# Kernel optimization log

Measured on AMD Instinct MI355X. Metric: run time of the kernel, lower is better.

Reference implementation:

```python
import jax, jax.numpy as jnp
import numpy as np

N = 500_000   # total nodes across the batch of graphs
D = 256       # node feature dim
G = 4096      # number of graphs (segments)


def setup_inputs() -> dict:
    key = jax.random.key(0)
    k1, k2, k3 = jax.random.split(key, 3)
    x = jax.random.normal(k1, (N, D), dtype=jnp.float32)
    batch = jnp.sort(jax.random.randint(k2, (N,), 0, G, dtype=jnp.int64))
    Wg = jax.random.normal(k3, (D,), dtype=jnp.float32) * (1.0 / np.sqrt(D))
    bg = jnp.zeros((1,), dtype=jnp.float32)
    return {"x": x, "batch": batch, "Wg": Wg, "bg": bg}


def reference(x, batch, Wg, bg):
    # gate_nn: Linear(D, 1), then squeeze -> [N]
    gate = x @ Wg + bg[0]
    # scatter_softmax over segments defined by batch
    gmax = jax.ops.segment_max(gate, batch, num_segments=G, indices_are_sorted=True)
    e = jnp.exp(gate - gmax[batch])
    denom = jax.ops.segment_sum(e, batch, num_segments=G, indices_are_sorted=True)
    attn = e / denom[batch]
    # weighted scatter-add pooling -> [G, D]
    out = jax.ops.segment_sum(x * attn[:, None], batch, num_segments=G,
                              indices_are_sorted=True)
    return out
```

## Files before the change

### kernel.cpp

```cpp
#include <hip/hip_runtime.h>
#include <math.h>


#define DIM 256

__device__ __forceinline__ int lower_bound(const int* __restrict__ b, int n, int key) {
    int lo = 0, hi = n;
    while (lo < hi) {
        int mid = (lo + hi) >> 1;
        if (b[mid] < key) lo = mid + 1; else hi = mid;
    }
    return lo;
}

__global__ __launch_bounds__(256)
void gap_fused_kernel(const float* __restrict__ x,
                      const int* __restrict__ batch,
                      const float* __restrict__ Wg,
                      const float* __restrict__ bg,
                      float* __restrict__ out,
                      int N) {
    const int g    = blockIdx.x;
    const int tid  = threadIdx.x;
    const int lane = tid & 63;
    const int wv   = tid >> 6;

    const int start = lower_bound(batch, N, g);
    const int end   = lower_bound(batch, N, g + 1);

    __shared__ float s_ml[8];
    __shared__ float s_acc[4 * DIM];

    if (start >= end) {
        out[(size_t)g * DIM + tid] = 0.0f;
        return;
    }

    const float4 wgv  = ((const float4*)Wg)[lane];
    const float  bias = bg[0];
    const int    len  = end - start;
    const float4* __restrict__ x4 = (const float4*)x + (size_t)start * (DIM / 4);

    float  m   = -INFINITY;
    float  l   = 0.0f;
    float4 acc = make_float4(0.f, 0.f, 0.f, 0.f);

    for (int r = wv; r < len; r += 8) {
        const int  r2   = r + 4;
        const bool has2 = (r2 < len);
        float4 v0 = x4[(size_t)r * 64 + lane];
        float4 v1 = make_float4(0.f, 0.f, 0.f, 0.f);
        if (has2) v1 = x4[(size_t)r2 * 64 + lane];

        float d0 = fmaf(v0.x, wgv.x, fmaf(v0.y, wgv.y, fmaf(v0.z, wgv.z, v0.w * wgv.w)));
        float d1 = fmaf(v1.x, wgv.x, fmaf(v1.y, wgv.y, fmaf(v1.z, wgv.z, v1.w * wgv.w)));
        #pragma unroll
        for (int off = 32; off; off >>= 1) {
            d0 += __shfl_xor(d0, off);
            d1 += __shfl_xor(d1, off);
        }
        const float g0 = d0 + bias;
        const float g1 = has2 ? (d1 + bias) : -INFINITY;

        const float nm    = fmaxf(m, fmaxf(g0, g1));
        const float alpha = __expf(m - nm);
        const float p0    = __expf(g0 - nm);
        const float p1    = __expf(g1 - nm);
        l = fmaf(l, alpha, p0 + p1);
        acc.x = fmaf(p0, v0.x, fmaf(p1, v1.x, acc.x * alpha));
        acc.y = fmaf(p0, v0.y, fmaf(p1, v1.y, acc.y * alpha));
        acc.z = fmaf(p0, v0.z, fmaf(p1, v1.z, acc.z * alpha));
        acc.w = fmaf(p0, v0.w, fmaf(p1, v1.w, acc.w * alpha));
        m = nm;
    }

    if (lane == 0) { s_ml[wv] = m; s_ml[4 + wv] = l; }
    ((float4*)s_acc)[wv * 64 + lane] = acc;
    __syncthreads();

    const float M = fmaxf(fmaxf(s_ml[0], s_ml[1]), fmaxf(s_ml[2], s_ml[3]));
    float denom = 0.f, val = 0.f;
    #pragma unroll
    for (int w = 0; w < 4; ++w) {
        const float sc = __expf(s_ml[w] - M);
        denom = fmaf(s_ml[4 + w], sc, denom);
        val   = fmaf(s_acc[w * DIM + tid], sc, val);
    }
    out[(size_t)g * DIM + tid] = val / denom;
}

extern "C" void kernel_launch(void* const* d_in, const int* in_sizes, int n_in,
                              void* d_out, int out_size, void* d_ws, size_t ws_size,
                              hipStream_t stream) {
    const float* x     = (const float*)d_in[0];
    const int*   batch = (const int*)d_in[1];
    const float* Wg    = (const float*)d_in[2];
    const float* bg    = (const float*)d_in[3];
    float*       out   = (float*)d_out;

    const int N = in_sizes[1];
    const int G = out_size / DIM;

    gap_fused_kernel<<<G, DIM, 0, stream>>>(x, batch, Wg, bg, out, N);
}
```

Before: 661.8 us.

## Precompute segment offsets and software-pipeline four rows per wave with prefetch

Adds a pre-pass kernel that builds segment offsets from the sorted batch array, replacing the per-block binary searches when workspace is available. The main loop now handles four rows per wave per iteration instead of two, and prefetches the next tile's rows into registers while computing the current one. It also skips the rescale exp when the running max does not change. This adds a second kernel launch and higher register pressure. Row indices are clamped, so the prefetch never reads past the segment, at the cost of some redundant loads on the last tile.

```diff
diff --git a/kernel.cpp b/kernel.cpp
--- a/kernel.cpp
+++ b/kernel.cpp
@@ -13,11 +13,30 @@
     return lo;
 }
 
+__global__ void build_offsets_kernel(const int* __restrict__ batch,
+                                     int* __restrict__ offs, int N, int G) {
+    int i = blockIdx.x * blockDim.x + threadIdx.x;
+    const int stride = gridDim.x * blockDim.x;
+    for (; i < N; i += stride) {
+        const int b    = batch[i];
+        const int prev = (i == 0) ? -1 : batch[i - 1];
+        for (int g = prev + 1; g <= b; ++g) offs[g] = i;
+        if (i == N - 1) {
+            for (int g = b + 1; g <= G; ++g) offs[g] = N;
+        }
+    }
+}
+
+__device__ __forceinline__ float dot4(const float4 a, const float4 b) {
+    return fmaf(a.x, b.x, fmaf(a.y, b.y, fmaf(a.z, b.z, a.w * b.w)));
+}
+
 __global__ __launch_bounds__(256)
 void gap_fused_kernel(const float* __restrict__ x,
                       const int* __restrict__ batch,
                       const float* __restrict__ Wg,
                       const float* __restrict__ bg,
+                      const int* __restrict__ offs,
                       float* __restrict__ out,
                       int N) {
     const int g    = blockIdx.x;
@@ -25,8 +44,14 @@
     const int lane = tid & 63;
     const int wv   = tid >> 6;
 
-    const int start = lower_bound(batch, N, g);
-    const int end   = lower_bound(batch, N, g + 1);
+    int start, end;
+    if (offs) {
+        start = offs[g];
+        end   = offs[g + 1];
+    } else {
+        start = lower_bound(batch, N, g);
+        end   = lower_bound(batch, N, g + 1);
+    }
 
     __shared__ float s_ml[8];
     __shared__ float s_acc[4 * DIM];
@@ -45,33 +70,63 @@
     float  l   = 0.0f;
     float4 acc = make_float4(0.f, 0.f, 0.f, 0.f);
 
-    for (int r = wv; r < len; r += 8) {
-        const int  r2   = r + 4;
-        const bool has2 = (r2 < len);
-        float4 v0 = x4[(size_t)r * 64 + lane];
-        float4 v1 = make_float4(0.f, 0.f, 0.f, 0.f);
-        if (has2) v1 = x4[(size_t)r2 * 64 + lane];
+    const int ntiles = (len + 15) >> 4;
+    const int rb     = wv * 4;
+    const int lmax   = len - 1;
 
-        float d0 = fmaf(v0.x, wgv.x, fmaf(v0.y, wgv.y, fmaf(v0.z, wgv.z, v0.w * wgv.w)));
-        float d1 = fmaf(v1.x, wgv.x, fmaf(v1.y, wgv.y, fmaf(v1.z, wgv.z, v1.w * wgv.w)));
+    auto ridx = [&](int row) -> size_t {
+        const int rr = row < lmax ? row : lmax;
+        return (size_t)rr * 64 + lane;
+    };
+
+    float4 c0 = x4[ridx(rb + 0)];
+    float4 c1 = x4[ridx(rb + 1)];
+    float4 c2 = x4[ridx(rb + 2)];
+    float4 c3 = x4[ridx(rb + 3)];
+
+    for (int j = 0; j < ntiles; ++j) {
+        const int base = j * 16 + rb;
+
+        const int nb = base + 16;
+        float4 n0 = x4[ridx(nb + 0)];
+        float4 n1 = x4[ridx(nb + 1)];
+        float4 n2 = x4[ridx(nb + 2)];
+        float4 n3 = x4[ridx(nb + 3)];
+
+        float d0 = dot4(c0, wgv);
+        float d1 = dot4(c1, wgv);
+        float d2 = dot4(c2, wgv);
+        float d3 = dot4(c3, wgv);
         #pragma unroll
         for (int off = 32; off; off >>= 1) {
             d0 += __shfl_xor(d0, off);
             d1 += __shfl_xor(d1, off);
+            d2 += __shfl_xor(d2, off);
+            d3 += __shfl_xor(d3, off);
         }
-        const float g0 = d0 + bias;
-        const float g1 = has2 ? (d1 + bias) : -INFINITY;
+        const bool v0 = (base + 0) < len;
+        const bool v1 = (base + 1) < len;
+        const bool v2 = (base + 2) < len;
+        const bool v3 = (base + 3) < len;
+        const float g0 = v0 ? d0 + bias : -INFINITY;
+        const float g1 = v1 ? d1 + bias : -INFINITY;
+        const float g2 = v2 ? d2 + bias : -INFINITY;
+        const float g3 = v3 ? d3 + bias : -INFINITY;
 
-        const float nm    = fmaxf(m, fmaxf(g0, g1));
-        const float alpha = __expf(m - nm);
-        const float p0    = __expf(g0 - nm);
-        const float p1    = __expf(g1 - nm);
-        l = fmaf(l, alpha, p0 + p1);
-        acc.x = fmaf(p0, v0.x, fmaf(p1, v1.x, acc.x * alpha));
-        acc.y = fmaf(p0, v0.y, fmaf(p1, v1.y, acc.y * alpha));
-        acc.z = fmaf(p0, v0.z, fmaf(p1, v1.z, acc.z * alpha));
-        acc.w = fmaf(p0, v0.w, fmaf(p1, v1.w, acc.w * alpha));
+        const float nm    = fmaxf(m, fmaxf(fmaxf(g0, g1), fmaxf(g2, g3)));
+        const float alpha = (m == nm) ? 1.0f : __expf(m - nm);
+        const float p0 = v0 ? __expf(g0 - nm) : 0.0f;
+        const float p1 = v1 ? __expf(g1 - nm) : 0.0f;
+        const float p2 = v2 ? __expf(g2 - nm) : 0.0f;
+        const float p3 = v3 ? __expf(g3 - nm) : 0.0f;
+        l = fmaf(l, alpha, (p0 + p1) + (p2 + p3));
+        acc.x = fmaf(p0, c0.x, fmaf(p1, c1.x, fmaf(p2, c2.x, fmaf(p3, c3.x, acc.x * alpha))));
+        acc.y = fmaf(p0, c0.y, fmaf(p1, c1.y, fmaf(p2, c2.y, fmaf(p3, c3.y, acc.y * alpha))));
+        acc.z = fmaf(p0, c0.z, fmaf(p1, c1.z, fmaf(p2, c2.z, fmaf(p3, c3.z, acc.z * alpha))));
+        acc.w = fmaf(p0, c0.w, fmaf(p1, c1.w, fmaf(p2, c2.w, fmaf(p3, c3.w, acc.w * alpha))));
         m = nm;
+
+        c0 = n0; c1 = n1; c2 = n2; c3 = n3;
     }
 
     if (lane == 0) { s_ml[wv] = m; s_ml[4 + wv] = l; }
@@ -101,5 +156,10 @@
     const int N = in_sizes[1];
     const int G = out_size / DIM;
 
-    gap_fused_kernel<<<G, DIM, 0, stream>>>(x, batch, Wg, bg, out, N);
+    int* offs = nullptr;
+    if (d_ws != nullptr && ws_size >= (size_t)(G + 1) * sizeof(int)) {
+        offs = (int*)d_ws;
+        build_offsets_kernel<<<1024, 256, 0, stream>>>(batch, offs, N, G);
+    }
+    gap_fused_kernel<<<G, DIM, 0, stream>>>(x, batch, Wg, bg, offs, out, N);
 }
```

Result: no change. 655.9 us (-0.9%).
